# Kernel optimization log

Measured on AMD Instinct MI355X. Metric: run time of the kernel, lower is better.

Reference implementation:

```python
import jax, jax.numpy as jnp
import numpy as np

B, T, D, H = 4, 1024, 1024, 16  # batch, seq, model dim (named head_size in source), n_heads


def setup_inputs() -> dict:
    key = jax.random.key(0)
    ks = jax.random.split(key, 12)
    s = 0.02
    x = jax.random.normal(ks[0], (B, T, D), jnp.float32)
    x1 = jax.random.normal(ks[1], (1,), jnp.float32)  # unused by module
    x2 = jax.random.normal(ks[2], (1,), jnp.float32)  # unused by module
    # bool mask, True = masked out; causal upper-triangular as typical usage
    attn_mask = jnp.triu(jnp.ones((T, T), dtype=bool), k=1)
    Wk = jax.random.normal(ks[3], (D, D), jnp.float32) * s
    bk = jax.random.normal(ks[4], (D,), jnp.float32) * s
    Wq = jax.random.normal(ks[5], (D, D), jnp.float32) * s
    bq = jax.random.normal(ks[6], (D,), jnp.float32) * s
    Wv = jax.random.normal(ks[7], (D, D), jnp.float32) * s
    bv = jax.random.normal(ks[8], (D,), jnp.float32) * s
    Wp = jax.random.normal(ks[9], (D, D), jnp.float32) * s
    bp = jax.random.normal(ks[10], (D,), jnp.float32) * s
    return {"x": x, "x1": x1, "x2": x2, "attn_mask": attn_mask,
            "Wk": Wk, "bk": bk, "Wq": Wq, "bq": bq,
            "Wv": Wv, "bv": bv, "Wp": Wp, "bp": bp}


def reference(x, x1, x2, attn_mask, Wk, bk, Wq, bq, Wv, bv, Wp, bp):
    b, t, c = x.shape
    n_heads = H
    hd = c // n_heads
    # torch nn.Linear: y = x @ W.T + b
    k = (x @ Wk.T + bk).reshape(b, t, n_heads, hd)
    q = (x @ Wq.T + bq).reshape(b, t, n_heads, hd)
    v = (x @ Wv.T + bv).reshape(b, t, n_heads, hd)
    scores = jnp.einsum('bkhi,bqhi->bkqh', k, q)  # [B,T(k),T(q),H]
    # mask BEFORE scaling (as in source; -inf is scale-invariant)
    scores = jnp.where(attn_mask[None, :t, :t, None], -jnp.inf, scores)
    scores = scores / jnp.sqrt(jnp.asarray(c, scores.dtype))  # scale by full model dim (source quirk)
    weights = jax.nn.softmax(scores, axis=2)  # softmax over QUERY axis (source quirk)
    out = jnp.einsum('bkqh,bqhj->bkhj', weights, v).reshape(b, t, c)
    out = out @ Wp.T + bp  # dropout p=0 -> identity
    return (out, weights)
```

## Files before the change

kernel.cpp:

```cpp
#include <hip/hip_runtime.h>
#include <cstdint>


typedef __bf16 bf16x8 __attribute__((ext_vector_type(8)));
typedef float  f32x4  __attribute__((ext_vector_type(4)));
using u16 = unsigned short;
using u32 = unsigned int;

__device__ __forceinline__ float bf2f(u16 u) {
  union { u32 u; float f; } x; x.u = ((u32)u) << 16; return x.f;
}
__device__ __forceinline__ u16 f2bf(float f) {
  union { float f; u32 u; } x; x.f = f;
  u32 u = x.u;
  return (u16)((u + 0x7fffu + ((u >> 16) & 1u)) >> 16);
}

__device__ __forceinline__ void storeC(float* p, float v) { *p = v; }
__device__ __forceinline__ void storeC(u16* p, float v)   { *p = f2bf(v); }

#define GLL(g, s) __builtin_amdgcn_global_load_lds(                      \
    (const __attribute__((address_space(1))) u32*)(g),                   \
    (__attribute__((address_space(3))) u32*)(s), 16, 0, 0)

__global__ __launch_bounds__(256) void cvt_f32_bf16(const float4* __restrict__ in,
                                                    uint2* __restrict__ out, int n4) {
  int i = blockIdx.x * 256 + threadIdx.x;
  if (i >= n4) return;
  float4 v = in[i];
  uint2 o;
  o.x = (u32)f2bf(v.x) | ((u32)f2bf(v.y) << 16);
  o.y = (u32)f2bf(v.z) | ((u32)f2bf(v.w) << 16);
  out[i] = o;
}

__global__ __launch_bounds__(256) void cvt_weights(const float4* __restrict__ w0,
                                                   const float4* __restrict__ w1,
                                                   const float4* __restrict__ w2,
                                                   const float4* __restrict__ w3,
                                                   uint2* __restrict__ out) {
  int which = blockIdx.y;
  const float4* src = (which == 0) ? w0 : (which == 1) ? w1 : (which == 2) ? w2 : w3;
  int i = blockIdx.x * 256 + threadIdx.x;
  float4 v = src[i];
  uint2 o;
  o.x = (u32)f2bf(v.x) | ((u32)f2bf(v.y) << 16);
  o.y = (u32)f2bf(v.z) | ((u32)f2bf(v.w) << 16);
  out[(size_t)which * 262144 + i] = o;
}

__global__ __launch_bounds__(256) void pack_bias(const float* __restrict__ b0,
                                                 const float* __restrict__ b1,
                                                 const float* __restrict__ b2,
                                                 float* __restrict__ out) {
  int t = blockIdx.x * 256 + threadIdx.x;
  const float* src = (t < 1024) ? b0 : (t < 2048) ? b1 : b2;
  out[t] = src[t & 1023];
}

template <typename CT>
__global__ __launch_bounds__(256) void gemm_nt(
    const u16* __restrict__ A, const u16* __restrict__ B,
    const float* __restrict__ bias, CT* __restrict__ C,
    int M, int N, int K, int lda, int ldb, int ldc,
    int nH, long long sAb, long long sAh, long long sBb, long long sBh,
    long long sCb, long long sCh, float alpha, int biasStrideH, int trimode)
{
  const int m0 = blockIdx.y * 128;
  const int n0 = blockIdx.x * 128;
  if (trimode == 1 && n0 > m0) return;

  int z = blockIdx.z;
  int bb = z / nH, hh = z % nH;
  A += bb * sAb + hh * sAh;
  B += bb * sBb + hh * sBh;
  C += bb * sCb + hh * sCh;

  __shared__ __align__(16) u16 As[128 * 32];
  __shared__ __align__(16) u16 Bs[128 * 32];

  const int t    = threadIdx.x;
  const int wave = t >> 6;
  const int lane = t & 63;

  const int r0 = (wave * 2 + 0) * 16 + (lane >> 2);
  const int r1 = (wave * 2 + 1) * 16 + (lane >> 2);
  const int cl = (lane & 3) * 8;
  const u16* aG0 = A + (size_t)(m0 + r0) * lda + cl;
  const u16* aG1 = A + (size_t)(m0 + r1) * lda + cl;
  const u16* bG0 = B + (size_t)(n0 + r0) * ldb + cl;
  const u16* bG1 = B + (size_t)(n0 + r1) * ldb + cl;
  u16* asD0 = As + (wave * 2 + 0) * 512;
  u16* asD1 = As + (wave * 2 + 1) * 512;
  u16* bsD0 = Bs + (wave * 2 + 0) * 512;
  u16* bsD1 = Bs + (wave * 2 + 1) * 512;

  const int wm = (wave >> 1) << 6;
  const int wn = (wave & 1) << 6;
  const int lr = lane & 15;
  const int lk = (lane >> 4) << 3;

  f32x4 acc[4][4];
  const f32x4 fzero = {0.f, 0.f, 0.f, 0.f};
#pragma unroll
  for (int i = 0; i < 4; i++)
#pragma unroll
    for (int j = 0; j < 4; j++) acc[i][j] = fzero;

  const int Kend = (trimode == 2) ? min(K, m0 + 128) : K;

  for (int k0 = 0; k0 < Kend; k0 += 32) {
    __syncthreads();
    GLL(aG0 + k0, asD0);
    GLL(aG1 + k0, asD1);
    GLL(bG0 + k0, bsD0);
    GLL(bG1 + k0, bsD1);
    __syncthreads();

    bf16x8 af[4], bf[4];
#pragma unroll
    for (int mi = 0; mi < 4; mi++)
      af[mi] = *(const bf16x8*)&As[(wm + mi * 16 + lr) * 32 + lk];
#pragma unroll
    for (int ni = 0; ni < 4; ni++)
      bf[ni] = *(const bf16x8*)&Bs[(wn + ni * 16 + lr) * 32 + lk];
#pragma unroll
    for (int mi = 0; mi < 4; mi++)
#pragma unroll
      for (int ni = 0; ni < 4; ni++)
        acc[mi][ni] = __builtin_amdgcn_mfma_f32_16x16x32_bf16(af[mi], bf[ni], acc[mi][ni], 0, 0, 0);
  }

  const int cr = (lane >> 4) << 2;
  const int cc = lane & 15;
#pragma unroll
  for (int mi = 0; mi < 4; mi++) {
#pragma unroll
    for (int ni = 0; ni < 4; ni++) {
      int gn = n0 + wn + ni * 16 + cc;
      if (gn >= N) continue;
      float bv = bias ? bias[biasStrideH * hh + gn] : 0.f;
      int gm = m0 + wm + mi * 16 + cr;
#pragma unroll
      for (int r = 0; r < 4; r++) {
        float v = acc[mi][ni][r] * alpha + bv;
        storeC(&C[(size_t)(gm + r) * ldc + gn], v);
      }
    }
  }
}

__global__ __launch_bounds__(256) void transpose_v(const u16* __restrict__ v, u16* __restrict__ vt) {
  __shared__ u16 tile[32][33];
  int z = blockIdx.z;
  int b = z >> 4, h = z & 15;
  int q0 = blockIdx.x * 32;
  int j0 = blockIdx.y * 32;
  int tx = threadIdx.x;
  int ty = threadIdx.y;
#pragma unroll
  for (int i = 0; i < 4; i++) {
    int r = ty + i * 8;
    tile[r][tx] = v[(size_t)(b * 1024 + q0 + r) * 1024 + h * 64 + j0 + tx];
  }
  __syncthreads();
#pragma unroll
  for (int i = 0; i < 4; i++) {
    int r = ty + i * 8;
    vt[(size_t)(z * 64 + j0 + r) * 1024 + q0 + tx] = tile[tx][r];
  }
}

__global__ __launch_bounds__(1024) void softmax_expand(u16* __restrict__ sw,
                                                       float* __restrict__ out_w) {
  __shared__ u32 lds[16 * 576];

  const int bk   = blockIdx.x;
  const int b    = bk >> 10, k = bk & 1023;
  const int w    = threadIdx.x >> 6;
  const int lane = threadIdx.x & 63;
  const int qb   = lane << 4;

  u16* row = sw + (((size_t)(b * 16 + w)) << 20) + ((size_t)k << 10);

  union { uint4 d; u16 s[8]; } a0, a1;
  if (qb <= k) {
    a0.d = *(const uint4*)(row + qb);
    a1.d = *(const uint4*)(row + qb + 8);
  } else {
    a0.d = make_uint4(0, 0, 0, 0);
    a1.d = make_uint4(0, 0, 0, 0);
  }

  float v[16];
  float mx = -INFINITY;
#pragma unroll
  for (int j = 0; j < 16; j++) {
    u16 raw = (j < 8) ? a0.s[j] : a1.s[j - 8];
    bool valid = (qb + j) <= k;
    v[j] = valid ? bf2f(raw) : -INFINITY;
    mx = fmaxf(mx, v[j]);
  }
#pragma unroll
  for (int o = 32; o > 0; o >>= 1) mx = fmaxf(mx, __shfl_xor(mx, o, 64));

  float sum = 0.f;
#pragma unroll
  for (int j = 0; j < 16; j++) {
    float e = ((qb + j) <= k) ? __expf(v[j] - mx) : 0.f;
    v[j] = e;
    sum += e;
  }
#pragma unroll
  for (int o = 32; o > 0; o >>= 1) sum += __shfl_xor(sum, o, 64);
  const float rinv = 1.f / sum;

#pragma unroll
  for (int j = 0; j < 8; j++) a0.s[j] = f2bf(v[j] * rinv);
#pragma unroll
  for (int j = 0; j < 8; j++) a1.s[j] = f2bf(v[j + 8] * rinv);

  if (qb <= (k | 127)) {
    *(uint4*)(row + qb)     = a0.d;
    *(uint4*)(row + qb + 8) = a1.d;
  }

  u32* run = &lds[w * 576 + lane * 9];
  run[0] = a0.d.x; run[1] = a0.d.y; run[2] = a0.d.z; run[3] = a0.d.w;
  run[4] = a1.d.x; run[5] = a1.d.y; run[6] = a1.d.z; run[7] = a1.d.w;
  __syncthreads();

  const int t    = threadIdx.x;
  const int Lr   = t >> 4;
  const int pr   = (t & 15) >> 1;
  const int half = (t & 1) << 4;

  float vals[16];
#pragma unroll
  for (int h = 0; h < 16; h++) {
    u32 packed = lds[h * 576 + Lr * 9 + pr];
    vals[h] = bf2f((u16)(packed >> half));
  }

  float4* o = (float4*)(out_w + (((size_t)bk << 10) + t) * 16);
  o[0] = make_float4(vals[0],  vals[1],  vals[2],  vals[3]);
  o[1] = make_float4(vals[4],  vals[5],  vals[6],  vals[7]);
  o[2] = make_float4(vals[8],  vals[9],  vals[10], vals[11]);
  o[3] = make_float4(vals[12], vals[13], vals[14], vals[15]);
}

extern "C" void kernel_launch(void* const* d_in, const int* in_sizes, int n_in,
                              void* d_out, int out_size, void* d_ws, size_t ws_size,
                              hipStream_t stream) {
  const float* x  = (const float*)d_in[0];
  const float* Wk = (const float*)d_in[4];
  const float* bk = (const float*)d_in[5];
  const float* Wq = (const float*)d_in[6];
  const float* bq = (const float*)d_in[7];
  const float* Wv = (const float*)d_in[8];
  const float* bv = (const float*)d_in[9];
  const float* Wp = (const float*)d_in[10];
  const float* bp = (const float*)d_in[11];

  float* out   = (float*)d_out;
  float* out_w = out + 4194304;

  u16* ws   = (u16*)d_ws;
  u16* xb   = ws;
  u16* wkb  = xb  + 4194304;
  u16* kbuf = wkb + 4194304;
  u16* vbuf = kbuf + 8388608;
  u16* vt   = kbuf + 12582912;
  u16* attn = vt   + 4194304;
  u16* sc   = attn + 4194304;
  float* bqkv = (float*)(sc + 67108864);

  cvt_f32_bf16<<<4096, 256, 0, stream>>>((const float4*)x, (uint2*)xb, 1048576);
  cvt_weights<<<dim3(1024, 4), 256, 0, stream>>>((const float4*)Wk, (const float4*)Wq,
                                                 (const float4*)Wv, (const float4*)Wp,
                                                 (uint2*)wkb);
  pack_bias<<<12, 256, 0, stream>>>(bk, bq, bv, bqkv);

  gemm_nt<u16><<<dim3(8, 32, 3), 256, 0, stream>>>(
      xb, wkb, bqkv, kbuf, 4096, 1024, 1024, 1024, 1024, 1024,
      3, 0, 0, 0, 1048576, 0, 4194304, 1.0f, 1024, 0);

  transpose_v<<<dim3(32, 2, 64), dim3(32, 8), 0, stream>>>(vbuf, vt);

  gemm_nt<u16><<<dim3(8, 8, 64), 256, 0, stream>>>(
      kbuf, kbuf + 4194304, nullptr, sc, 1024, 1024, 64, 1024, 1024, 1024,
      16, 1048576, 64, 1048576, 64, 16777216, 1048576, 0.03125f, 0, 1);

  softmax_expand<<<4096, 1024, 0, stream>>>(sc, out_w);

  gemm_nt<u16><<<dim3(1, 8, 64), 256, 0, stream>>>(
      sc, vt, nullptr, attn, 1024, 64, 1024, 1024, 1024, 1024,
      16, 16777216, 1048576, 1048576, 65536, 1048576, 64, 1.0f, 0, 2);

  gemm_nt<float><<<dim3(8, 32, 1), 256, 0, stream>>>(
      attn, wkb + 3145728, bp, out, 4096, 1024, 1024, 1024, 1024, 1024,
      1, 0, 0, 0, 0, 0, 0, 1.0f, 0, 0);
}
```

Before: 552.7 us.

## Fuse score GEMM, exponentiation and PV GEMM into one attention kernel

Replaces the separate QK^T GEMM, softmax kernel and PV GEMM with a fused kernel that computes scores per 128-key block, exponentiates them without max subtraction, accumulates row sums and multiplies by V in the same loop. It writes unnormalized bf16 probabilities plus per-row sums, and the expand kernel then normalizes while transposing into the fp32 weights output. The input and weight conversion kernels are also merged into one launch. Skipping the max subtraction cuts a pass over the score matrix, but it relies on the scaled scores staying small enough that exp does not overflow.

```diff
diff --git a/kernel.cpp b/kernel.cpp
--- a/kernel.cpp
+++ b/kernel.cpp
@@ -23,30 +23,24 @@
     (const __attribute__((address_space(1))) u32*)(g),                   \
     (__attribute__((address_space(3))) u32*)(s), 16, 0, 0)
 
-__global__ __launch_bounds__(256) void cvt_f32_bf16(const float4* __restrict__ in,
-                                                    uint2* __restrict__ out, int n4) {
+__global__ __launch_bounds__(256) void cvt_all(const float4* __restrict__ x,
+                                               const float4* __restrict__ wk,
+                                               const float4* __restrict__ wq,
+                                               const float4* __restrict__ wv,
+                                               const float4* __restrict__ wp,
+                                               uint2* __restrict__ out) {
   int i = blockIdx.x * 256 + threadIdx.x;
-  if (i >= n4) return;
-  float4 v = in[i];
+  const float4* src; int off;
+  if (i < 1048576) { src = x; off = i; }
+  else {
+    int j = i - 1048576; int w = j >> 18; off = j & 262143;
+    src = (w == 0) ? wk : (w == 1) ? wq : (w == 2) ? wv : wp;
+  }
+  float4 v = src[off];
   uint2 o;
   o.x = (u32)f2bf(v.x) | ((u32)f2bf(v.y) << 16);
   o.y = (u32)f2bf(v.z) | ((u32)f2bf(v.w) << 16);
   out[i] = o;
-}
-
-__global__ __launch_bounds__(256) void cvt_weights(const float4* __restrict__ w0,
-                                                   const float4* __restrict__ w1,
-                                                   const float4* __restrict__ w2,
-                                                   const float4* __restrict__ w3,
-                                                   uint2* __restrict__ out) {
-  int which = blockIdx.y;
-  const float4* src = (which == 0) ? w0 : (which == 1) ? w1 : (which == 2) ? w2 : w3;
-  int i = blockIdx.x * 256 + threadIdx.x;
-  float4 v = src[i];
-  uint2 o;
-  o.x = (u32)f2bf(v.x) | ((u32)f2bf(v.y) << 16);
-  o.y = (u32)f2bf(v.z) | ((u32)f2bf(v.w) << 16);
-  out[(size_t)which * 262144 + i] = o;
 }
 
 __global__ __launch_bounds__(256) void pack_bias(const float* __restrict__ b0,
@@ -64,11 +58,10 @@
     const float* __restrict__ bias, CT* __restrict__ C,
     int M, int N, int K, int lda, int ldb, int ldc,
     int nH, long long sAb, long long sAh, long long sBb, long long sBh,
-    long long sCb, long long sCh, float alpha, int biasStrideH, int trimode)
+    long long sCb, long long sCh, float alpha, int biasStrideH)
 {
   const int m0 = blockIdx.y * 128;
   const int n0 = blockIdx.x * 128;
-  if (trimode == 1 && n0 > m0) return;
 
   int z = blockIdx.z;
   int bb = z / nH, hh = z % nH;
@@ -107,9 +100,7 @@
 #pragma unroll
     for (int j = 0; j < 4; j++) acc[i][j] = fzero;
 
-  const int Kend = (trimode == 2) ? min(K, m0 + 128) : K;
-
-  for (int k0 = 0; k0 < Kend; k0 += 32) {
+  for (int k0 = 0; k0 < K; k0 += 32) {
     __syncthreads();
     GLL(aG0 + k0, asD0);
     GLL(aG1 + k0, asD1);
@@ -171,8 +162,177 @@
   }
 }
 
-__global__ __launch_bounds__(1024) void softmax_expand(u16* __restrict__ sw,
-                                                       float* __restrict__ out_w) {
+__global__ __launch_bounds__(256, 2) void fused_attn(
+    const u16* __restrict__ kq,
+    const u16* __restrict__ vt,
+    u16* __restrict__ sc, u16* __restrict__ attn, float* __restrict__ lbuf)
+{
+  const int kb = 7 - blockIdx.x;
+  const int bh = blockIdx.y;
+  const int b  = bh >> 4, h = bh & 15;
+  const int k0 = kb << 7;
+
+  __shared__ __align__(16) u16 Kl[128 * 72];
+  __shared__ __align__(16) u16 QV[128 * 72];
+  __shared__ __align__(16) u16 Pl[128 * 136];
+  __shared__ float l_sm[2][128];
+
+  const int t    = threadIdx.x;
+  const int wave = t >> 6, lane = t & 63;
+  const int wm = (wave >> 1) << 6, wn = (wave & 1) << 6;
+  const int lr = lane & 15, lk = (lane >> 4) << 3;
+  const int cr = (lane >> 4) << 2, cc = lane & 15;
+
+  {
+    const int r = t >> 1, cb = (t & 1) << 5;
+    const u16* g = kq + (size_t)(b * 1024 + k0 + r) * 1024 + h * 64 + cb;
+    u16* d = Kl + r * 72 + cb;
+#pragma unroll
+    for (int i = 0; i < 4; i++)
+      *(uint4*)(d + i * 8) = *(const uint4*)(g + i * 8);
+  }
+
+  const u16* qbase = kq + 4194304 + (size_t)(b * 1024) * 1024 + h * 64;
+  const u16* vbase = vt + (size_t)(bh * 64) * 1024;
+
+  f32x4 oacc[2][4];
+  const f32x4 fz = {0.f, 0.f, 0.f, 0.f};
+#pragma unroll
+  for (int i = 0; i < 2; i++)
+#pragma unroll
+    for (int j = 0; j < 4; j++) oacc[i][j] = fz;
+  float lsum[4][4] = {};
+
+  const int qr = t >> 1, qcb = (t & 1) << 5;
+  const int vr = t >> 2, vcb = (t & 3) << 5;
+
+  for (int tq = 0; tq <= kb; tq++) {
+    const int q0 = tq << 7;
+    uint4 qreg[4], vreg[4];
+    const u16* qg = qbase + (size_t)(q0 + qr) * 1024 + qcb;
+    const u16* vg = vbase + (size_t)vr * 1024 + q0 + vcb;
+#pragma unroll
+    for (int i = 0; i < 4; i++) qreg[i] = *(const uint4*)(qg + i * 8);
+#pragma unroll
+    for (int i = 0; i < 4; i++) vreg[i] = *(const uint4*)(vg + i * 8);
+
+    __syncthreads();
+    {
+      u16* d = QV + qr * 72 + qcb;
+#pragma unroll
+      for (int i = 0; i < 4; i++) *(uint4*)(d + i * 8) = qreg[i];
+    }
+    __syncthreads();
+
+    f32x4 sacc[4][4];
+#pragma unroll
+    for (int i = 0; i < 4; i++)
+#pragma unroll
+      for (int j = 0; j < 4; j++) sacc[i][j] = fz;
+#pragma unroll
+    for (int ks = 0; ks < 2; ks++) {
+      bf16x8 af[4], bf[4];
+#pragma unroll
+      for (int mi = 0; mi < 4; mi++)
+        af[mi] = *(const bf16x8*)&Kl[(wm + mi * 16 + lr) * 72 + ks * 32 + lk];
+#pragma unroll
+      for (int ni = 0; ni < 4; ni++)
+        bf[ni] = *(const bf16x8*)&QV[(wn + ni * 16 + lr) * 72 + ks * 32 + lk];
+#pragma unroll
+      for (int mi = 0; mi < 4; mi++)
+#pragma unroll
+        for (int ni = 0; ni < 4; ni++)
+          sacc[mi][ni] = __builtin_amdgcn_mfma_f32_16x16x32_bf16(af[mi], bf[ni], sacc[mi][ni], 0, 0, 0);
+    }
+    __syncthreads();
+
+#pragma unroll
+    for (int mi = 0; mi < 4; mi++) {
+#pragma unroll
+      for (int ni = 0; ni < 4; ni++) {
+        const int col = wn + ni * 16 + cc;
+#pragma unroll
+        for (int r = 0; r < 4; r++) {
+          const int row = wm + mi * 16 + cr + r;
+          bool valid = (q0 + col) <= (k0 + row);
+          float e = valid ? __expf(sacc[mi][ni][r] * 0.03125f) : 0.f;
+          lsum[mi][r] += e;
+          u32 bb = f2bf(e);
+          u32 ob = (u32)__shfl_xor((int)bb, 1, 64);
+          if ((lane & 1) == 0)
+            *(u32*)&Pl[row * 136 + (col & ~1)] = bb | (ob << 16);
+        }
+      }
+    }
+    {
+      u16* d = QV + vr * 136 + vcb;
+#pragma unroll
+      for (int i = 0; i < 4; i++) *(uint4*)(d + i * 8) = vreg[i];
+    }
+    __syncthreads();
+
+#pragma unroll
+    for (int ks = 0; ks < 4; ks++) {
+      bf16x8 pa[2], vb[4];
+#pragma unroll
+      for (int mi = 0; mi < 2; mi++)
+        pa[mi] = *(const bf16x8*)&Pl[(wave * 32 + mi * 16 + lr) * 136 + ks * 32 + lk];
+#pragma unroll
+      for (int ni = 0; ni < 4; ni++)
+        vb[ni] = *(const bf16x8*)&QV[(ni * 16 + lr) * 136 + ks * 32 + lk];
+#pragma unroll
+      for (int mi = 0; mi < 2; mi++)
+#pragma unroll
+        for (int ni = 0; ni < 4; ni++)
+          oacc[mi][ni] = __builtin_amdgcn_mfma_f32_16x16x32_bf16(pa[mi], vb[ni], oacc[mi][ni], 0, 0, 0);
+    }
+    {
+      const int r = t >> 1, cb2 = (t & 1) << 6;
+      u16* g = sc + ((size_t)bh << 20) + (size_t)(k0 + r) * 1024 + q0 + cb2;
+      const u16* s = Pl + r * 136 + cb2;
+#pragma unroll
+      for (int i = 0; i < 8; i++) *(uint4*)(g + i * 8) = *(const uint4*)(s + i * 8);
+    }
+  }
+
+#pragma unroll
+  for (int mi = 0; mi < 4; mi++)
+#pragma unroll
+    for (int r = 0; r < 4; r++) {
+      float v = lsum[mi][r];
+#pragma unroll
+      for (int o = 1; o < 16; o <<= 1) v += __shfl_xor(v, o, 64);
+      lsum[mi][r] = v;
+    }
+  __syncthreads();
+  if ((lane & 15) == 0) {
+#pragma unroll
+    for (int mi = 0; mi < 4; mi++)
+#pragma unroll
+      for (int r = 0; r < 4; r++)
+        l_sm[wave & 1][wm + mi * 16 + cr + r] = lsum[mi][r];
+  }
+  __syncthreads();
+  if (t < 128)
+    lbuf[(size_t)bh * 1024 + k0 + t] = l_sm[0][t] + l_sm[1][t];
+
+#pragma unroll
+  for (int mi = 0; mi < 2; mi++) {
+#pragma unroll
+    for (int r = 0; r < 4; r++) {
+      const int row = wave * 32 + mi * 16 + cr + r;
+      const float rinv = 1.f / (l_sm[0][row] + l_sm[1][row]);
+#pragma unroll
+      for (int ni = 0; ni < 4; ni++)
+        attn[(size_t)(b * 1024 + k0 + row) * 1024 + h * 64 + ni * 16 + cc] =
+            f2bf(oacc[mi][ni][r] * rinv);
+    }
+  }
+}
+
+__global__ __launch_bounds__(1024) void expand_norm(const u16* __restrict__ sw,
+                                                    const float* __restrict__ lbuf,
+                                                    float* __restrict__ out_w) {
   __shared__ u32 lds[16 * 576];
 
   const int bk   = blockIdx.x;
@@ -181,7 +341,8 @@
   const int lane = threadIdx.x & 63;
   const int qb   = lane << 4;
 
-  u16* row = sw + (((size_t)(b * 16 + w)) << 20) + ((size_t)k << 10);
+  const float rinv = 1.f / lbuf[(size_t)(b * 16 + w) * 1024 + k];
+  const u16* row = sw + (((size_t)(b * 16 + w)) << 20) + ((size_t)k << 10);
 
   union { uint4 d; u16 s[8]; } a0, a1;
   if (qb <= k) {
@@ -192,42 +353,17 @@
     a1.d = make_uint4(0, 0, 0, 0);
   }
 
-  float v[16];
-  float mx = -INFINITY;
+  u16 outp[16];
 #pragma unroll
   for (int j = 0; j < 16; j++) {
     u16 raw = (j < 8) ? a0.s[j] : a1.s[j - 8];
-    bool valid = (qb + j) <= k;
-    v[j] = valid ? bf2f(raw) : -INFINITY;
-    mx = fmaxf(mx, v[j]);
-  }
-#pragma unroll
-  for (int o = 32; o > 0; o >>= 1) mx = fmaxf(mx, __shfl_xor(mx, o, 64));
-
-  float sum = 0.f;
-#pragma unroll
-  for (int j = 0; j < 16; j++) {
-    float e = ((qb + j) <= k) ? __expf(v[j] - mx) : 0.f;
-    v[j] = e;
-    sum += e;
-  }
-#pragma unroll
-  for (int o = 32; o > 0; o >>= 1) sum += __shfl_xor(sum, o, 64);
-  const float rinv = 1.f / sum;
-
-#pragma unroll
-  for (int j = 0; j < 8; j++) a0.s[j] = f2bf(v[j] * rinv);
-#pragma unroll
-  for (int j = 0; j < 8; j++) a1.s[j] = f2bf(v[j + 8] * rinv);
-
-  if (qb <= (k | 127)) {
-    *(uint4*)(row + qb)     = a0.d;
-    *(uint4*)(row + qb + 8) = a1.d;
+    float e = ((qb + j) <= k) ? bf2f(raw) * rinv : 0.f;
+    outp[j] = f2bf(e);
   }
 
   u32* run = &lds[w * 576 + lane * 9];
-  run[0] = a0.d.x; run[1] = a0.d.y; run[2] = a0.d.z; run[3] = a0.d.w;
-  run[4] = a1.d.x; run[5] = a1.d.y; run[6] = a1.d.z; run[7] = a1.d.w;
+#pragma unroll
+  for (int j = 0; j < 8; j++) run[j] = (u32)outp[2 * j] | ((u32)outp[2 * j + 1] << 16);
   __syncthreads();
 
   const int t    = threadIdx.x;
@@ -274,30 +410,23 @@
   u16* attn = vt   + 4194304;
   u16* sc   = attn + 4194304;
   float* bqkv = (float*)(sc + 67108864);
-
-  cvt_f32_bf16<<<4096, 256, 0, stream>>>((const float4*)x, (uint2*)xb, 1048576);
-  cvt_weights<<<dim3(1024, 4), 256, 0, stream>>>((const float4*)Wk, (const float4*)Wq,
-                                                 (const float4*)Wv, (const float4*)Wp,
-                                                 (uint2*)wkb);
+  float* lbuf = bqkv + 3072;
+
+  cvt_all<<<8192, 256, 0, stream>>>((const float4*)x, (const float4*)Wk, (const float4*)Wq,
+                                    (const float4*)Wv, (const float4*)Wp, (uint2*)ws);
   pack_bias<<<12, 256, 0, stream>>>(bk, bq, bv, bqkv);
 
   gemm_nt<u16><<<dim3(8, 32, 3), 256, 0, stream>>>(
       xb, wkb, bqkv, kbuf, 4096, 1024, 1024, 1024, 1024, 1024,
-      3, 0, 0, 0, 1048576, 0, 4194304, 1.0f, 1024, 0);
+      3, 0, 0, 0, 1048576, 0, 4194304, 1.0f, 1024);
 
   transpose_v<<<dim3(32, 2, 64), dim3(32, 8), 0, stream>>>(vbuf, vt);
 
-  gemm_nt<u16><<<dim3(8, 8, 64), 256, 0, stream>>>(
-      kbuf, kbuf + 4194304, nullptr, sc, 1024, 1024, 64, 1024, 1024, 1024,
-      16, 1048576, 64, 1048576, 64, 16777216, 1048576, 0.03125f, 0, 1);
-
-  softmax_expand<<<4096, 1024, 0, stream>>>(sc, out_w);
-
-  gemm_nt<u16><<<dim3(1, 8, 64), 256, 0, stream>>>(
-      sc, vt, nullptr, attn, 1024, 64, 1024, 1024, 1024, 1024,
-      16, 16777216, 1048576, 1048576, 65536, 1048576, 64, 1.0f, 0, 2);
+  fused_attn<<<dim3(8, 64), 256, 0, stream>>>(kbuf, vt, sc, attn, lbuf);
+
+  expand_norm<<<4096, 1024, 0, stream>>>(sc, lbuf, out_w);
 
   gemm_nt<float><<<dim3(8, 32, 1), 256, 0, stream>>>(
       attn, wkb + 3145728, bp, out, 4096, 1024, 1024, 1024, 1024, 1024,
-      1, 0, 0, 0, 0, 0, 0, 1.0f, 0, 0);
-}
+      1, 0, 0, 0, 0, 0, 0, 1.0f, 0);
+}
```

Measured after the change: 549.5 us. Within noise of the previous version (-0.6%).
